# Kernel tuning notes

Hardware: AMD Instinct MI355X
Metric: run time of the kernel (lower is better)

## Reference

```python
import jax, jax.numpy as jnp
import numpy as np

EMBED = 768
B, S = 8, 2048

def setup_inputs() -> dict:
    key = jax.random.key(0)
    k1, k2, k3, k4 = jax.random.split(key, 4)
    x = jax.random.normal(k1, (B, S, EMBED), dtype=jnp.float32)
    scale = 1.0 / np.sqrt(EMBED)
    Wv = jax.random.normal(k2, (EMBED, EMBED), dtype=jnp.float32) * scale
    Wk = jax.random.normal(k3, (EMBED, EMBED), dtype=jnp.float32) * scale
    Wq = jax.random.normal(k4, (EMBED, EMBED), dtype=jnp.float32) * scale
    mask = jnp.ones((B, S, S), dtype=jnp.int32)
    return {"x": x, "Wv": Wv, "Wk": Wk, "Wq": Wq, "mask": mask}

def reference(x, Wv, Wk, Wq, mask):
    # nn.Linear(E, E, bias=False): y = x @ W.T
    values = jnp.einsum('bse,fe->bsf', x, Wv)
    keys = jnp.einsum('bse,fe->bsf', x, Wk)
    queries = jnp.einsum('bse,fe->bsf', x, Wq)
    energy = jnp.einsum('bqd,bkd->bqk', queries, keys)  # [B,S,S]
    energy = jnp.where(mask == 0, jnp.float32(-1e20), energy)
    attention = jax.nn.softmax(energy / jnp.sqrt(jnp.float32(EMBED)), axis=2)
    out = jnp.einsum('bqk,bkd->bqd', attention, values)
    return out
```

## Files before the change

### kernel.cpp

```cpp
#include <hip/hip_runtime.h>
#include <stdint.h>

#define EMB 768
#define NBATCH 8
#define SEQ 2048
#define M_TOT (NBATCH*SEQ)

using bf16x8 = __attribute__((ext_vector_type(8))) short;
using f32x4  = __attribute__((ext_vector_type(4))) float;

__device__ __forceinline__ short f2bf(float f) {
  __bf16 h = (__bf16)f;
  return __builtin_bit_cast(short, h);
}
__device__ __forceinline__ f32x4 MFMA(bf16x8 a, bf16x8 b, f32x4 c) {
  return __builtin_amdgcn_mfma_f32_16x16x32_bf16(a, b, c, 0, 0, 0);
}
#define GLOAD_LDS16(g, l) __builtin_amdgcn_global_load_lds( \
    (const __attribute__((address_space(1))) unsigned int*)(g), \
    (__attribute__((address_space(3))) unsigned int*)(l), 16, 0, 0)

__device__ __forceinline__ unsigned spread4(unsigned x) {
  x = (x | (x << 12)) & 0x000F000Fu;
  x = (x | (x << 6))  & 0x03030303u;
  x = (x | (x << 3))  & 0x11111111u;
  return x;
}

__global__ __launch_bounds__(256) void cvt_xw(
    const float* __restrict__ x, const float* __restrict__ Wq,
    const float* __restrict__ Wk, const float* __restrict__ Wv,
    short* __restrict__ xb, short* __restrict__ Wb)
{
  const size_t NXU = (size_t)M_TOT * EMB / 8;
  const size_t NWU = (size_t)EMB * EMB / 8;
  const size_t total = NXU + 3 * NWU;
  for (size_t u = (size_t)blockIdx.x * 256 + threadIdx.x; u < total;
       u += (size_t)gridDim.x * 256) {
    const float* src; short* dst; size_t off;
    if (u < NXU)            { src = x;  dst = xb;                     off = u; }
    else if (u < NXU+NWU)   { src = Wq; dst = Wb;                     off = u - NXU; }
    else if (u < NXU+2*NWU) { src = Wk; dst = Wb + (size_t)EMB*EMB;   off = u - NXU - NWU; }
    else                    { src = Wv; dst = Wb + (size_t)2*EMB*EMB; off = u - NXU - 2*NWU; }
    float4 a = reinterpret_cast<const float4*>(src)[off*2];
    float4 c = reinterpret_cast<const float4*>(src)[off*2+1];
    bf16x8 o;
    o[0]=f2bf(a.x); o[1]=f2bf(a.y); o[2]=f2bf(a.z); o[3]=f2bf(a.w);
    o[4]=f2bf(c.x); o[5]=f2bf(c.y); o[6]=f2bf(c.z); o[7]=f2bf(c.w);
    reinterpret_cast<bf16x8*>(dst)[off] = o;
  }
}

#define STAGE_128(As, Bs, asrc, bsrc, lda, ldb)                              \
  {                                                                          \
    _Pragma("unroll")                                                        \
    for (int i = 0; i < 4; ++i) {                                            \
      int slot = i*256 + t;                                                  \
      int row = slot >> 3, g = slot & 7;                                     \
      int gs = (g ^ (row & 7)) << 3;                                         \
      GLOAD_LDS16((asrc) + (size_t)row*(lda) + gs,                           \
                  (char*)&As[0] + (size_t)(i*256 + w*64)*16);                \
      GLOAD_LDS16((bsrc) + (size_t)row*(ldb) + gs,                           \
                  (char*)&Bs[0] + (size_t)(i*256 + w*64)*16);                \
    }                                                                        \
  }

#define MFMA_128(As, Bs)                                                     \
  {                                                                          \
    _Pragma("unroll")                                                        \
    for (int ks = 0; ks < 2; ++ks) {                                         \
      bf16x8 a[4], bb[4];                                                    \
      _Pragma("unroll")                                                      \
      for (int i = 0; i < 4; ++i) {                                          \
        int ra = wm*64 + i*16 + l15;                                         \
        a[i]  = *reinterpret_cast<const bf16x8*>(                            \
                  &As[ra*64 + (((ks*4 + l4) ^ (ra & 7)) << 3)]);             \
        int rb = wn*64 + i*16 + l15;                                         \
        bb[i] = *reinterpret_cast<const bf16x8*>(                            \
                  &Bs[rb*64 + (((ks*4 + l4) ^ (rb & 7)) << 3)]);             \
      }                                                                      \
      _Pragma("unroll")                                                      \
      for (int mi = 0; mi < 4; ++mi)                                         \
        _Pragma("unroll")                                                    \
        for (int ni = 0; ni < 4; ++ni)                                       \
          acc[mi][ni] = MFMA(a[mi], bb[ni], acc[mi][ni]);                    \
    }                                                                        \
  }

__global__ __launch_bounds__(256, 4) void qkv_gemm(
    const short* __restrict__ xb, const short* __restrict__ Wb,
    const int* __restrict__ mask,
    short* __restrict__ Qb, short* __restrict__ Kb, short* __restrict__ Vt,
    unsigned int* __restrict__ bits)
{
  __shared__ short As[128*64];
  __shared__ short Bs[128*64];

  const int bid = blockIdx.x;
  const int nb = (bid & 7) * 288 + (bid >> 3);
  const int g = nb / 12, r = nb % 12;
  const int bm = (g / 6) * 4 + r / 3;
  const int bn = (g % 6) * 3 + r % 3;
  const int mbase = bm * 128;

  const short* asrc = xb + (size_t)mbase * EMB;
  const short* bsrc = Wb + (size_t)bn * 128 * EMB;

  const int t = threadIdx.x, lane = t & 63, w = t >> 6;
  const int wm = w >> 1, wn = w & 1, l15 = lane & 15, l4 = lane >> 4;

  f32x4 acc[4][4] = {};

  STAGE_128(As, Bs, asrc, bsrc, EMB, EMB);
  for (int kk = 0; kk < 12; ++kk) {
    asm volatile("s_waitcnt vmcnt(0)" ::: "memory");
    __syncthreads();
    MFMA_128(As, Bs);
    if (kk < 11) {
      __syncthreads();
      STAGE_128(As, Bs, asrc + (kk+1)*64, bsrc + (kk+1)*64, EMB, EMB);
    }
  }

#pragma unroll
  for (int mi = 0; mi < 4; ++mi) {
#pragma unroll
    for (int ni = 0; ni < 4; ++ni) {
      int f = bn * 128 + wn * 64 + ni * 16 + l15;
      int m0 = mbase + wm * 64 + mi * 16 + l4 * 4;
      f32x4 v = acc[mi][ni];
      if (f < 1536) {
        short* dst = (f < 768) ? (Qb + f) : (Kb + (f - 768));
#pragma unroll
        for (int j = 0; j < 4; ++j)
          dst[(size_t)(m0 + j) * EMB] = f2bf(v[j]);
      } else {
        int f2 = f - 1536, bb2 = m0 >> 11, s = m0 & 2047;
        short4 pk = make_short4(f2bf(v[0]), f2bf(v[1]), f2bf(v[2]), f2bf(v[3]));
        *reinterpret_cast<short4*>(&Vt[((size_t)bb2 * EMB + f2) * SEQ + s]) = pk;
      }
    }
  }

  {
    const int gw = bid * 4 + w;
    for (int row = gw; row < M_TOT; row += 2304 * 4) {
      const int4* row4 = reinterpret_cast<const int4*>(mask + (size_t)row * SEQ);
      int4 v[8];
#pragma unroll
      for (int i = 0; i < 8; ++i) v[i] = row4[i*64 + lane];
      unsigned long long sel0 = 0, sel1 = 0, sel2 = 0, sel3 = 0;
      const int grp = lane >> 3;
#pragma unroll
      for (int i = 0; i < 8; ++i) {
        unsigned long long b0 = __ballot(v[i].x != 0);
        unsigned long long b1 = __ballot(v[i].y != 0);
        unsigned long long b2 = __ballot(v[i].z != 0);
        unsigned long long b3 = __ballot(v[i].w != 0);
        if (grp == i) { sel0 = b0; sel1 = b1; sel2 = b2; sel3 = b3; }
      }
      const int sh = (lane & 7) * 8;
      unsigned wrd = spread4((unsigned)(sel0 >> sh) & 0xffu)
                   | (spread4((unsigned)(sel1 >> sh) & 0xffu) << 1)
                   | (spread4((unsigned)(sel2 >> sh) & 0xffu) << 2)
                   | (spread4((unsigned)(sel3 >> sh) & 0xffu) << 3);
      bits[(size_t)row * 64 + lane] = wrd;
    }
  }
}

#define STAGE_HALF(ldsb, src, ld, k0, h)                                      \
  { _Pragma("unroll") for (int i_ = 0; i_ < 2; ++i_) {                        \
      int slot_ = i_*512 + t;                                                 \
      int row_ = (h)*128 + (slot_ >> 3), g_ = slot_ & 7;                      \
      GLOAD_LDS16((src) + (size_t)row_*(ld) + (k0) + ((g_ ^ (row_ & 7)) << 3),\
                  (ldsb) + (h)*16384 + (size_t)(i_*512 + w*64)*16); } }

#define READ_A(mh)                                                            \
  _Pragma("unroll") for (int ks_ = 0; ks_ < 2; ++ks_)                         \
    _Pragma("unroll") for (int mi_ = 0; mi_ < 4; ++mi_) {                     \
      int r_ = (mh)*128 + wm*64 + mi_*16 + l15;                               \
      a_c[ks_][mi_] = *reinterpret_cast<const bf16x8*>(                       \
          Ar + r_*64 + (((ks_*4 + l4) ^ (r_ & 7)) << 3));                     \
    }

#define READ_B(nh)                                                            \
  _Pragma("unroll") for (int ks_ = 0; ks_ < 2; ++ks_)                         \
    _Pragma("unroll") for (int ni_ = 0; ni_ < 2; ++ni_) {                     \
      int r_ = (nh)*128 + wn*32 + ni_*16 + l15;                               \
      b_c[nh][ks_][ni_] = *reinterpret_cast<const bf16x8*>(                   \
          Br + r_*64 + (((ks_*4 + l4) ^ (r_ & 7)) << 3));                     \
    }

#define PHASE(mh, nh, W, RD, ...)                                             \
  {                                                                           \
    RD                                                                        \
    __VA_ARGS__                                                               \
    asm volatile("s_waitcnt vmcnt(" #W ")" ::: "memory");                     \
    asm volatile("s_barrier" ::: "memory");                                   \
    __builtin_amdgcn_s_setprio(1);                                            \
    _Pragma("unroll") for (int ks_ = 0; ks_ < 2; ++ks_)                       \
      _Pragma("unroll") for (int mi_ = 0; mi_ < 4; ++mi_)                     \
        _Pragma("unroll") for (int ni_ = 0; ni_ < 2; ++ni_)                   \
          acc[mh][nh][mi_][ni_] =                                             \
              MFMA(a_c[ks_][mi_], b_c[nh][ks_][ni_], acc[mh][nh][mi_][ni_]);  \
    __builtin_amdgcn_s_setprio(0);                                            \
    asm volatile("s_barrier" ::: "memory");                                   \
  }

#define GEMM_PRO_BODY(asrc, bsrc, lda, ldb, NT)                               \
  short* const A0p = (short*)smem;                                            \
  short* const B0p = (short*)(smem + 32768);                                  \
  short* const A1p = (short*)(smem + 65536);                                  \
  short* const B1p = (short*)(smem + 98304);                                  \
  f32x4 acc[2][2][4][2] = {};                                                 \
  bf16x8 a_c[2][4], b_c[2][2][2];                                             \
  STAGE_HALF((char*)A0p, asrc, lda, 0, 0);                                    \
  STAGE_HALF((char*)B0p, bsrc, ldb, 0, 0);                                    \
  STAGE_HALF((char*)B0p, bsrc, ldb, 0, 1);                                    \
  STAGE_HALF((char*)A0p, asrc, lda, 0, 1);                                    \
  asm volatile("s_waitcnt vmcnt(4)" ::: "memory");                            \
  asm volatile("s_barrier" ::: "memory");                                     \
  for (int T = 0; T < (NT) - 1; ++T) {                                        \
    short* Ar = (T & 1) ? A1p : A0p;                                          \
    short* Br = (T & 1) ? B1p : B0p;                                          \
    char* Aw = (char*)((T & 1) ? A0p : A1p);                                  \
    char* Bw = (char*)((T & 1) ? B0p : B1p);                                  \
    const int nk = (T + 1) * 64;                                              \
    PHASE(0,0, 4, READ_A(0) READ_B(0), STAGE_HALF(Aw, asrc, lda, nk, 0))      \
    PHASE(0,1, 4, READ_B(1),           STAGE_HALF(Bw, bsrc, ldb, nk, 0))      \
    PHASE(1,0, 4, READ_A(1),           STAGE_HALF(Bw, bsrc, ldb, nk, 1))      \
    PHASE(1,1, 4, ,                    STAGE_HALF(Aw, asrc, lda, nk, 1))      \
  }                                                                           \
  {                                                                           \
    short* Ar = (((NT)-1) & 1) ? A1p : A0p;                                   \
    short* Br = (((NT)-1) & 1) ? B1p : B0p;                                   \
    asm volatile("s_waitcnt vmcnt(0)" ::: "memory");         \
    asm volatile("s_barrier" ::: "memory");                                   \
    PHASE(0,0, 0, READ_A(0) READ_B(0), )                                      \
    PHASE(0,1, 0, READ_B(1), )                                                \
    PHASE(1,0, 0, READ_A(1), )                                                \
    PHASE(1,1, 0, , )                                                         \
  }

__global__ __launch_bounds__(512, 2) void energy(
    const short* __restrict__ Qb, const short* __restrict__ Kb,
    const unsigned int* __restrict__ bitw, short* __restrict__ S,
    float* __restrict__ partial)
{
  extern __shared__ char smem[];
  const int t = threadIdx.x, lane = t & 63, w = t >> 6;
  const int wm = w >> 2, wn = w & 3, l15 = lane & 15, l4 = lane >> 4;

  const int bid = blockIdx.x;
  const int nb = (bid & 7) * 64 + (bid >> 3);
  const int b = nb >> 6;
  const int idx = nb & 63;
  const int sup = idx >> 2, sub = idx & 3;
  const int qt = (sup >> 2) * 2 + (sub >> 1);
  const int kt = (sup & 3) * 2 + (sub & 1);

  const short* asrc = Qb + ((size_t)b*SEQ + qt*256) * EMB;
  const short* bsrc = Kb + ((size_t)b*SEQ + kt*256) * EMB;

  GEMM_PRO_BODY(asrc, bsrc, EMB, EMB, 12)

  const float SCL = 1.4426950408889634f / 27.712812921102035f;
  short* srow = S + (size_t)b * SEQ * SEQ;

  float rsum[2][4][4];
#pragma unroll
  for (int mh = 0; mh < 2; ++mh)
#pragma unroll
    for (int mi = 0; mi < 4; ++mi)
#pragma unroll
      for (int j = 0; j < 4; ++j) rsum[mh][mi][j] = 0.f;

#pragma unroll
  for (int mh = 0; mh < 2; ++mh)
#pragma unroll
  for (int mi = 0; mi < 4; ++mi)
#pragma unroll
  for (int j = 0; j < 4; ++j) {
    int q = qt*256 + mh*128 + wm*64 + mi*16 + l4*4 + j;
    size_t qg = (size_t)b*SEQ + q;
#pragma unroll
    for (int nh = 0; nh < 2; ++nh) {
      unsigned int wrd = bitw[qg*64 + kt*8 + nh*4 + wn];
#pragma unroll
      for (int ni = 0; ni < 2; ++ni) {
        float p = ((wrd >> (ni*16 + l15)) & 1u)
                    ? __builtin_amdgcn_exp2f(acc[mh][nh][mi][ni][j] * SCL) : 0.f;
        srow[(size_t)q*SEQ + kt*256 + nh*128 + wn*32 + ni*16 + l15] = f2bf(p);
        rsum[mh][mi][j] += p;
      }
    }
  }
#pragma unroll
  for (int off = 8; off >= 1; off >>= 1)
#pragma unroll
    for (int mh = 0; mh < 2; ++mh)
#pragma unroll
      for (int mi = 0; mi < 4; ++mi)
#pragma unroll
        for (int j = 0; j < 4; ++j)
          rsum[mh][mi][j] += __shfl_xor(rsum[mh][mi][j], off);

  float* sm = (float*)smem;
  if (l15 == 0) {
#pragma unroll
    for (int mh = 0; mh < 2; ++mh)
#pragma unroll
      for (int mi = 0; mi < 4; ++mi)
#pragma unroll
        for (int j = 0; j < 4; ++j)
          sm[wn*256 + mh*128 + wm*64 + mi*16 + l4*4 + j] = rsum[mh][mi][j];
  }
  __syncthreads();
  if (t < 256) {
    float s4 = (sm[t] + sm[256+t]) + (sm[512+t] + sm[768+t]);
    partial[(size_t)kt*M_TOT + b*SEQ + qt*256 + t] = s4;
  }
}

__global__ __launch_bounds__(256) void lred(
    const float* __restrict__ partial, float* __restrict__ invl)
{
  int i = blockIdx.x * 256 + threadIdx.x;
  float s = 0.f;
#pragma unroll
  for (int kt = 0; kt < 8; ++kt) s += partial[(size_t)kt*M_TOT + i];
  invl[i] = 1.0f / s;
}

__global__ __launch_bounds__(512, 2) void pv(
    const short* __restrict__ P, const short* __restrict__ Vt,
    const float* __restrict__ invl, float* __restrict__ out)
{
  extern __shared__ char smem[];
  const int t = threadIdx.x, lane = t & 63, w = t >> 6;
  const int wm = w >> 2, wn = w & 3, l15 = lane & 15, l4 = lane >> 4;

  const int bid = blockIdx.x;
  const int nb = (bid & 7) * 24 + (bid >> 3);
  const int b = nb / 24;
  const int idx = nb % 24;
  const int qt = idx / 3, dt = idx % 3;

  const short* asrc = P  + ((size_t)b*SEQ + qt*256) * SEQ;
  const short* bsrc = Vt + ((size_t)b*EMB + dt*256) * SEQ;

  GEMM_PRO_BODY(asrc, bsrc, SEQ, SEQ, 32)

#pragma unroll
  for (int mh = 0; mh < 2; ++mh)
#pragma unroll
  for (int nh = 0; nh < 2; ++nh)
#pragma unroll
  for (int mi = 0; mi < 4; ++mi)
#pragma unroll
  for (int j = 0; j < 4; ++j) {
    int q = qt*256 + mh*128 + wm*64 + mi*16 + l4*4 + j;
    float il = invl[b*SEQ + q];
    float* orow = out + ((size_t)b*SEQ + q) * EMB;
#pragma unroll
    for (int ni = 0; ni < 2; ++ni) {
      int d = dt*256 + nh*128 + wn*32 + ni*16 + l15;
      orow[d] = acc[mh][nh][mi][ni][j] * il;
    }
  }
}

extern "C" void kernel_launch(void* const* d_in, const int* in_sizes, int n_in,
                              void* d_out, int out_size, void* d_ws, size_t ws_size,
                              hipStream_t stream)
{
  (void)in_sizes; (void)n_in; (void)out_size; (void)ws_size;
  const float* x  = (const float*)d_in[0];
  const float* Wv = (const float*)d_in[1];
  const float* Wk = (const float*)d_in[2];
  const float* Wq = (const float*)d_in[3];
  const int* mask = (const int*)d_in[4];
  float* out = (float*)d_out;

  short* Qb = (short*)d_ws;
  short* Kb = Qb + (size_t)M_TOT * EMB;
  short* Vt = Kb + (size_t)M_TOT * EMB;
  short* S  = Vt + (size_t)M_TOT * EMB;
  float* partial = (float*)(S + (size_t)NBATCH * SEQ * SEQ);
  float* invl = partial + (size_t)8 * M_TOT;
  short* xb = S;
  short* Wb = S + (size_t)M_TOT * EMB;
  unsigned int* bits = (unsigned int*)d_out;

  cvt_xw<<<dim3(2048), dim3(256), 0, stream>>>(x, Wq, Wk, Wv, xb, Wb);
  qkv_gemm<<<dim3(2304), dim3(256), 0, stream>>>(xb, Wb, mask, Qb, Kb, Vt, bits);
  energy<<<dim3(512), dim3(512), 131072, stream>>>(Qb, Kb, bits, S, partial);
  lred<<<dim3(64), dim3(256), 0, stream>>>(partial, invl);
  pv<<<dim3(192), dim3(512), 131072, stream>>>(S, Vt, invl, out);
}
```

Baseline: 229.7 us.

## Interleave mask bit-packing loads with the QKV projection GEMM k-loop

The mask-to-bitmask conversion used to run after the projection GEMM epilogue, loading all eight int4 chunks of each row at once. It is now spread across the GEMM k-loop: one mask chunk is loaded and ballot-reduced per iteration, and a second row is staged from iteration 3 onward. The goal is to hide the large mask read behind the MFMA work instead of running it as a separate memory-bound tail. The catch is that the per-iteration vmcnt(0) wait now also waits on these mask loads, which can stall the GEMM pipeline. Register pressure also rises from the extra carried state.

After: 322.7 us. +40.5%, slower.

```diff
diff --git a/kernel.cpp b/kernel.cpp
--- a/kernel.cpp
+++ b/kernel.cpp
@@ -109,6 +109,17 @@
   const int t = threadIdx.x, lane = t & 63, w = t >> 6;
   const int wm = w >> 1, wn = w & 1, l15 = lane & 15, l4 = lane >> 4;
 
+  const int gw = bid * 4 + w;
+  const int row2 = gw + 9216;
+  const bool has2 = (row2 < M_TOT);
+  const int4* r1 = reinterpret_cast<const int4*>(mask + (size_t)gw * SEQ);
+  const int4* r2 = reinterpret_cast<const int4*>(mask + (size_t)row2 * SEQ);
+  const int grp = lane >> 3;
+  unsigned long long s10=0, s11=0, s12=0, s13=0;
+  unsigned long long s20=0, s21=0, s22=0, s23=0;
+  int4 v1, v2;
+  v1 = r1[lane];
+
   f32x4 acc[4][4] = {};
 
   STAGE_128(As, Bs, asrc, bsrc, EMB, EMB);
@@ -116,6 +127,25 @@
     asm volatile("s_waitcnt vmcnt(0)" ::: "memory");
     __syncthreads();
     MFMA_128(As, Bs);
+
+    if (kk < 8) {
+      unsigned long long b0 = __ballot(v1.x != 0);
+      unsigned long long b1 = __ballot(v1.y != 0);
+      unsigned long long b2 = __ballot(v1.z != 0);
+      unsigned long long b3 = __ballot(v1.w != 0);
+      if (grp == kk) { s10 = b0; s11 = b1; s12 = b2; s13 = b3; }
+      if (kk < 7) v1 = r1[(kk+1)*64 + lane];
+    }
+    if (kk >= 4 && has2) {
+      unsigned long long b0 = __ballot(v2.x != 0);
+      unsigned long long b1 = __ballot(v2.y != 0);
+      unsigned long long b2 = __ballot(v2.z != 0);
+      unsigned long long b3 = __ballot(v2.w != 0);
+      if (grp == kk-4) { s20 = b0; s21 = b1; s22 = b2; s23 = b3; }
+    }
+    if (kk >= 3 && kk < 11 && has2)
+      v2 = r2[(kk-3)*64 + lane];
+
     if (kk < 11) {
       __syncthreads();
       STAGE_128(As, Bs, asrc + (kk+1)*64, bsrc + (kk+1)*64, EMB, EMB);
@@ -143,28 +173,18 @@
   }
 
   {
-    const int gw = bid * 4 + w;
-    for (int row = gw; row < M_TOT; row += 2304 * 4) {
-      const int4* row4 = reinterpret_cast<const int4*>(mask + (size_t)row * SEQ);
-      int4 v[8];
-#pragma unroll
-      for (int i = 0; i < 8; ++i) v[i] = row4[i*64 + lane];
-      unsigned long long sel0 = 0, sel1 = 0, sel2 = 0, sel3 = 0;
-      const int grp = lane >> 3;
-#pragma unroll
-      for (int i = 0; i < 8; ++i) {
-        unsigned long long b0 = __ballot(v[i].x != 0);
-        unsigned long long b1 = __ballot(v[i].y != 0);
-        unsigned long long b2 = __ballot(v[i].z != 0);
-        unsigned long long b3 = __ballot(v[i].w != 0);
-        if (grp == i) { sel0 = b0; sel1 = b1; sel2 = b2; sel3 = b3; }
-      }
-      const int sh = (lane & 7) * 8;
-      unsigned wrd = spread4((unsigned)(sel0 >> sh) & 0xffu)
-                   | (spread4((unsigned)(sel1 >> sh) & 0xffu) << 1)
-                   | (spread4((unsigned)(sel2 >> sh) & 0xffu) << 2)
-                   | (spread4((unsigned)(sel3 >> sh) & 0xffu) << 3);
-      bits[(size_t)row * 64 + lane] = wrd;
+    const int sh = (lane & 7) * 8;
+    unsigned w1 = spread4((unsigned)(s10 >> sh) & 0xffu)
+                | (spread4((unsigned)(s11 >> sh) & 0xffu) << 1)
+                | (spread4((unsigned)(s12 >> sh) & 0xffu) << 2)
+                | (spread4((unsigned)(s13 >> sh) & 0xffu) << 3);
+    bits[(size_t)gw * 64 + lane] = w1;
+    if (has2) {
+      unsigned w2 = spread4((unsigned)(s20 >> sh) & 0xffu)
+                  | (spread4((unsigned)(s21 >> sh) & 0xffu) << 1)
+                  | (spread4((unsigned)(s22 >> sh) & 0xffu) << 2)
+                  | (spread4((unsigned)(s23 >> sh) & 0xffu) << 3);
+      bits[(size_t)row2 * 64 + lane] = w2;
     }
   }
 }
```
